# Optimization experiments

Measured on AMD Instinct MI355X. Metric: run time of the kernel, lower is better.

## Reference

```python
import jax, jax.numpy as jnp
import numpy as np

EPS = 1e-6
NEG = 0.2  # leaky-relu negative slope
OBJ_C = 6

def _knn(x, k):
    # x: [B,3,N] -> [B,N,k] indices of k nearest neighbors (incl. self)
    xx = jnp.sum(x * x, axis=1)
    inner = jnp.einsum('bdn,bdm->bnm', x, x)
    pd = 2.0 * inner - xx[:, :, None] - xx[:, None, :]  # negative sq dist
    return jax.lax.top_k(pd, k)[1]

def _gather_pts(xt, idx):
    # xt [B,N,D], idx [B,N,k] -> [B,N,k,D]
    return xt[jnp.arange(xt.shape[0])[:, None, None], idx]

def _vn_lin(W, x):
    # channel-mixing linear over VN channel dim: x [B,Cin,3,...]
    return jnp.einsum('oc,bc...->bo...', W, x)

def _vn_bn(x, g, b, eps=1e-5):
    # VNBatchNorm with batch statistics on vector norms
    n = jnp.linalg.norm(x, axis=2) + EPS          # [B,C,*spatial]
    axes = (0,) + tuple(range(2, n.ndim))
    m = jnp.mean(n, axes, keepdims=True)
    v = jnp.var(n, axes, keepdims=True)
    shp = (1, -1) + (1,) * (n.ndim - 2)
    nb = g.reshape(shp) * (n - m) / jnp.sqrt(v + eps) + b.reshape(shp)
    return x / n[:, :, None] * nb[:, :, None]

def _vn_leaky(p, d):
    dot = jnp.sum(p * d, axis=2, keepdims=True)
    dsq = jnp.sum(d * d, axis=2, keepdims=True)
    return NEG * p + (1.0 - NEG) * jnp.where(dot >= 0, p, p - (dot / (dsq + EPS)) * d)

def _vn_block(x, wf, wd, g=None, b=None):
    # VNLinearLeakyReLU
    p = _vn_lin(wf, x)
    if g is not None:
        p = _vn_bn(p, g, b)
    return _vn_leaky(p, _vn_lin(wd, x))

def _surface_feature(coord, k):
    # coord [B,3,N] -> [B,3(chan),3(vec),N,k]: (nb-ctr, ctr, nb x ctr)
    idx = _knn(coord, k)
    xt = coord.transpose(0, 2, 1)                                  # [B,N,3]
    nb = _gather_pts(xt, idx)[:, :, :, None, :]                    # [B,N,k,1,3]
    ctr = jnp.broadcast_to(xt[:, :, None, None, :], nb.shape)
    f = jnp.concatenate([nb - ctr, ctr, jnp.cross(nb, ctr, axis=-1)], axis=3)
    return f.transpose(0, 3, 4, 1, 2)

def _neighbor_feature(x, coord, k):
    # x [B,C,3,N], knn over coord -> [B,C,3,N,k]
    B, C, _, N = x.shape
    idx = _knn(coord, k)
    xt = x.reshape(B, C * 3, N).transpose(0, 2, 1)                 # [B,N,C*3]
    f = _gather_pts(xt, idx).reshape(B, N, k, C, 3)
    return f.transpose(0, 3, 4, 1, 2)

def _vn_maxpool_down(x, coord, wd, rate):
    # x [B,C,3,N,k]: stride-subsample points, VN-max over k neighbors
    x = x[:, :, :, ::rate, :]
    coord_d = coord[:, :, ::rate]
    dot = jnp.sum(x * _vn_lin(wd, x), axis=2)                      # [B,C,Nd,k]
    idx = jnp.argmax(dot, axis=-1)
    xm = jnp.take_along_axis(x, idx[:, :, None, :, None], axis=-1)[..., 0]
    return xm, coord_d

def _nearest_index(t, s):
    # t [B,N,3], s [B,M,3] -> argmin sq-dist index [B,N]
    d = jnp.sum(t * t, -1)[:, :, None] - 2.0 * jnp.einsum('bnd,bmd->bnm', t, s) + jnp.sum(s * s, -1)[:, None, :]
    return jnp.argmin(d, axis=-1)

def _index_points(x, idx):
    # x [B,C,3,M], idx [B,N] -> [B,C,3,N]
    xt = x.transpose(0, 3, 1, 2)
    return xt[jnp.arange(x.shape[0])[:, None], idx].transpose(0, 2, 3, 1)

def _conv_bn_relu(x, w, b, g, be, eps=1e-5):
    # 1x1 Conv1d + BatchNorm1d (batch stats) + ReLU
    y = jnp.einsum('oc,bcn->bon', w, x) + b[None, :, None]
    m = jnp.mean(y, (0, 2), keepdims=True)
    v = jnp.var(y, (0, 2), keepdims=True)
    return jax.nn.relu(g[None, :, None] * (y - m) / jnp.sqrt(v + eps) + be[None, :, None])

def _forward(x, norm, cat_id, wf0, wd0, g0, b0, wf1, wd1, g1, b1, wp1, wf2, wd2, g2, b2, wf3, wd3, g3, b3, wp2, wf4, wd4, g4, b4, wv1f, wv1d, wv2f, wv2d, w3, ws1, cb1, sg1, sb1, ws2, cb2, sg2, sb2, ws3, cb3, sg3, sb3):
    B, _, _, N = x.shape
    coord = x.reshape(B, 3, N)
    one_hot = jax.nn.one_hot(cat_id, OBJ_C, dtype=x.dtype)
    x0 = _vn_block(_surface_feature(coord, 20), wf0, wd0, g0, b0).mean(-1)   # [B,42,3,N]
    x1 = _vn_block(x0, wf1, wd1, g1, b1)
    x2, coord2 = _vn_maxpool_down(_neighbor_feature(x1, coord, 4), coord, wp1, 4)
    x2 = _vn_block(x2, wf2, wd2, g2, b2)                                     # [B,84,3,N/4]
    x3 = _vn_block(x2, wf3, wd3, g3, b3)
    x4, coord4 = _vn_maxpool_down(_neighbor_feature(x3, coord2, 4), coord2, wp2, 4)
    x4 = _vn_block(x4, wf4, wd4, g4, b4)                                     # [B,168,3,N/16]
    ct = coord.transpose(0, 2, 1)
    i1 = _nearest_index(ct, coord2.transpose(0, 2, 1))
    i2 = _nearest_index(ct, coord4.transpose(0, 2, 1))
    eqv = jnp.concatenate([x0, x1, _index_points(x2, i1), _index_points(x3, i1), _index_points(x4, i2)], axis=1)  # [B,420,3,N]
    mean_feat = eqv.mean(-1, keepdims=True)                                  # [B,420,3,1]
    z = _vn_block(mean_feat, wv1f, wv1d)
    z = _vn_block(z, wv2f, wv2d)
    z = jnp.einsum('bcvm,kc->bvkm', z, w3)                                   # [B,3,2,1]
    inv_gl = jnp.einsum('bijm,bjkm->bikm', mean_feat, z).reshape(B, -1, 1)   # [B,840,1]
    inv_0 = jnp.broadcast_to(inv_gl, (B, inv_gl.shape[1], N))
    inv_1 = jnp.sum(mean_feat * coord[:, None], axis=2)                      # [B,420,N]
    oh = jnp.broadcast_to(one_hot[:, :, None], (B, OBJ_C, N))
    inv = jnp.concatenate([norm, inv_0, inv_1, oh], axis=1)                  # [B,1267,N]
    inv = _conv_bn_relu(inv, ws1, cb1, sg1, sb1)
    inv = _conv_bn_relu(inv, ws2, cb2, sg2, sb2)
    inv = _conv_bn_relu(inv, ws3, cb3, sg3, sb3)                             # [B,420,N]
    return eqv, mean_feat, inv, inv_gl

def setup_inputs():
    key = jax.random.key(0)
    ki = iter(jax.random.split(key, 40))
    B, N, D = 4, 2048, 42
    def lin(o, c):
        return jax.random.normal(next(ki), (o, c), jnp.float32) / float(np.sqrt(c))
    inp = dict(
        x=jax.random.normal(next(ki), (B, 1, 3, N), jnp.float32),
        norm=jax.random.normal(next(ki), (B, 1, N), jnp.float32),
        cat_id=jax.random.randint(next(ki), (B,), 0, OBJ_C),
        wf0=lin(D, 3), wd0=lin(D, 3), g0=jnp.ones(D), b0=jnp.zeros(D),
        wf1=lin(D, D), wd1=lin(D, D), g1=jnp.ones(D), b1=jnp.zeros(D),
        wp1=lin(D, D),
        wf2=lin(2 * D, D), wd2=lin(2 * D, D), g2=jnp.ones(2 * D), b2=jnp.zeros(2 * D),
        wf3=lin(2 * D, 2 * D), wd3=lin(2 * D, 2 * D), g3=jnp.ones(2 * D), b3=jnp.zeros(2 * D),
        wp2=lin(2 * D, 2 * D),
        wf4=lin(4 * D, 2 * D), wd4=lin(4 * D, 2 * D), g4=jnp.ones(4 * D), b4=jnp.zeros(4 * D),
        wv1f=lin(5 * D, 10 * D), wv1d=lin(5 * D, 10 * D),
        wv2f=lin(2 * D, 5 * D), wv2d=lin(2 * D, 5 * D),
        w3=lin(2, 2 * D),
        ws1=lin(1024, 1267), cb1=jnp.zeros(1024), sg1=jnp.ones(1024), sb1=jnp.zeros(1024),
        ws2=lin(512, 1024), cb2=jnp.zeros(512), sg2=jnp.ones(512), sb2=jnp.zeros(512),
        ws3=lin(420, 512), cb3=jnp.zeros(420), sg3=jnp.ones(420), sb3=jnp.zeros(420),
    )
    return inp

def reference(x, norm, cat_id, wf0, wd0, g0, b0, wf1, wd1, g1, b1, wp1, wf2, wd2, g2, b2, wf3, wd3, g3, b3, wp2, wf4, wd4, g4, b4, wv1f, wv1d, wv2f, wv2d, w3, ws1, cb1, sg1, sb1, ws2, cb2, sg2, sb2, ws3, cb3, sg3, sb3):
    return _forward(x, norm, cat_id, wf0, wd0, g0, b0, wf1, wd1, g1, b1, wp1, wf2, wd2, g2, b2, wf3, wd3, g3, b3, wp2, wf4, wd4, g4, b4, wv1f, wv1d, wv2f, wv2d, w3, ws1, cb1, sg1, sb1, ws2, cb2, sg2, sb2, ws3, cb3, sg3, sb3)
```

## Files before the change

kernel.cpp:

```cpp
#include <hip/hip_runtime.h>
#include <hip/hip_bf16.h>
#include <cstdint>
#include <cstddef>

#define NTOT 2048
#define BTOT 4

typedef short bf16x8 __attribute__((ext_vector_type(8)));
typedef float f32x4 __attribute__((ext_vector_type(4)));

__device__ inline unsigned short f2b(float v) {
    __hip_bfloat16 h = __float2bfloat16(v);
    return *reinterpret_cast<unsigned short*>(&h);
}

static const size_t WS_IDX20 = 0;
static const size_t WS_X0    = 1638400;
static const size_t WS_X1    = 3702784;
static const size_t WS_XM2   = 5767168;
static const size_t WS_X2    = 6025216;
static const size_t WS_X3    = 6541312;
static const size_t WS_IDX42 = 7057408;
static const size_t WS_XM4   = 7059456;
static const size_t WS_X4    = 7188480;
static const size_t WS_I1    = 7446528;
static const size_t WS_I2    = 7454720;
static const size_t WS_MF    = 7462912;
static const size_t WS_INVGL = 7467952;
static const size_t WS_STATS = 7471312;
static const size_t WS_CST   = 7472992;
static const size_t WS_CB    = 7480320;
static const size_t WS_AB    = 7484416;
static const size_t WS_W0    = 7496704;
static const size_t WS_Z1    = 7497728;
static const size_t WS_Z2    = 7500288;
static const size_t WS_W2B   = 13378560;
static const size_t WS_W3B   = 13640704;
static const size_t WS_Y1B   = 0;
static const size_t WS_Y2T   = 7480320;
static const size_t WS_Y2B   = 4194304;
static const size_t WS_Y3T   = 13771776;

#define ST0_OFF 0
#define ST1_OFF 84
#define ST2_OFF 168
#define ST3_OFF 336
#define ST4_OFF 504
#define CST1_OFF 0
#define CST2_OFF 2048
#define CST3_OFF 3072

#define OUT_EQV   0
#define OUT_MF    10321920
#define OUT_INV   10326960
#define OUT_INVGL 13767600

template <int SLOTS, int K, int NQ>
__global__ __launch_bounds__(256)
void knn_reg_kernel(const float* __restrict__ coord, int cand_stride, int q_stride,
                    int* __restrict__ out_idx, int q_cnt)
{
#pragma clang fp contract(off)
    constexpr int Q = SLOTS / 8;
    int b = blockIdx.y;
    int wave = threadIdx.x >> 6, lane = threadIdx.x & 63;
    int qbase = (blockIdx.x * 4 + wave) * NQ;
    if (qbase >= q_cnt) return;
    float qx[NQ], qy[NQ], qz[NQ], xxq[NQ];
#pragma unroll
    for (int u = 0; u < NQ; ++u) {
        int nq = (qbase + u) * q_stride;
        qx[u] = coord[(b * 3 + 0) * NTOT + nq];
        qy[u] = coord[(b * 3 + 1) * NTOT + nq];
        qz[u] = coord[(b * 3 + 2) * NTOT + nq];
        xxq[u] = qx[u] * qx[u] + qy[u] * qy[u] + qz[u] * qz[u];
    }
    float v[NQ][SLOTS];
#pragma unroll
    for (int j = 0; j < SLOTS; ++j) {
        int mo = (lane + 64 * j) * cand_stride;
        float cx = coord[(b * 3 + 0) * NTOT + mo];
        float cy = coord[(b * 3 + 1) * NTOT + mo];
        float cz = coord[(b * 3 + 2) * NTOT + mo];
        float xxc = cx * cx + cy * cy + cz * cz;
#pragma unroll
        for (int u = 0; u < NQ; ++u) {
            float inner = qx[u] * cx + qy[u] * cy + qz[u] * cz;
            v[u][j] = (2.0f * inner - xxq[u]) - xxc;
        }
    }
    float qv[NQ][Q]; int qj[NQ][Q];
#pragma unroll
    for (int u = 0; u < NQ; ++u)
#pragma unroll
        for (int qq = 0; qq < Q; ++qq) {
            float nv = v[u][qq * 8]; int nj = qq * 8;
#pragma unroll
            for (int j = 1; j < 8; ++j)
                if (v[u][qq * 8 + j] > nv) { nv = v[u][qq * 8 + j]; nj = qq * 8 + j; }
            qv[u][qq] = nv; qj[u][qq] = nj;
        }
#pragma clang loop unroll(disable)
    for (int kk = 0; kk < K; ++kk) {
        float bv[NQ]; int bm[NQ];
#pragma unroll
        for (int u = 0; u < NQ; ++u) {
            float tv = qv[u][0]; int tj = qj[u][0];
#pragma unroll
            for (int qq = 1; qq < Q; ++qq)
                if (qv[u][qq] > tv) { tv = qv[u][qq]; tj = qj[u][qq]; }
            bv[u] = tv; bm[u] = lane + 64 * tj;
        }
        for (int off = 32; off; off >>= 1) {
            float ov[NQ]; int om[NQ];
#pragma unroll
            for (int u = 0; u < NQ; ++u) {
                ov[u] = __shfl_down(bv[u], off);
                om[u] = __shfl_down(bm[u], off);
            }
#pragma unroll
            for (int u = 0; u < NQ; ++u)
                if (ov[u] > bv[u] || (ov[u] == bv[u] && om[u] < bm[u])) {
                    bv[u] = ov[u]; bm[u] = om[u];
                }
        }
#pragma unroll
        for (int u = 0; u < NQ; ++u) {
            int m_win = __builtin_amdgcn_readfirstlane(bm[u]);
            if (lane == 0)
                out_idx[((size_t)(b * q_cnt) + qbase + u) * K + kk] = m_win;
            int w_slot = m_win >> 6;
            bool isw = (lane == (m_win & 63));
#pragma unroll
            for (int qq = 0; qq < Q; ++qq) {
                if (qq == (w_slot >> 3)) {
#pragma unroll
                    for (int j = 0; j < 8; ++j)
                        if (qq * 8 + j == w_slot)
                            v[u][qq * 8 + j] = isw ? -3.4e38f : v[u][qq * 8 + j];
                    float nv = v[u][qq * 8]; int nj = qq * 8;
#pragma unroll
                    for (int j = 1; j < 8; ++j)
                        if (v[u][qq * 8 + j] > nv) { nv = v[u][qq * 8 + j]; nj = qq * 8 + j; }
                    qv[u][qq] = nv; qj[u][qq] = nj;
                }
            }
        }
    }
}

template <int SLOTS>
__global__ __launch_bounds__(256)
void nearest_reg_kernel(const float* __restrict__ coord, int cand_stride,
                        int* __restrict__ out)
{
#pragma clang fp contract(off)
    int b = blockIdx.y;
    int wave = threadIdx.x >> 6, lane = threadIdx.x & 63;
    int n = blockIdx.x * 4 + wave;
    float qx = coord[(b * 3 + 0) * NTOT + n];
    float qy = coord[(b * 3 + 1) * NTOT + n];
    float qz = coord[(b * 3 + 2) * NTOT + n];
    float tt = qx * qx + qy * qy + qz * qz;
    float v[SLOTS];
#pragma unroll
    for (int j = 0; j < SLOTS; ++j) {
        int mo = (lane + 64 * j) * cand_stride;
        float cx = coord[(b * 3 + 0) * NTOT + mo];
        float cy = coord[(b * 3 + 1) * NTOT + mo];
        float cz = coord[(b * 3 + 2) * NTOT + mo];
        float inner = qx * cx + qy * cy + qz * cz;
        float ss = cx * cx + cy * cy + cz * cz;
        v[j] = (tt - 2.0f * inner) + ss;
    }
    float bv = v[0];
    int bj = 0;
#pragma unroll
    for (int j = 1; j < SLOTS; ++j)
        if (v[j] < bv) { bv = v[j]; bj = j; }
    int bm = lane + 64 * bj;
    for (int off = 32; off; off >>= 1) {
        float ov = __shfl_down(bv, off);
        int   om = __shfl_down(bm, off);
        if (ov < bv || (ov == bv && om < bm)) { bv = ov; bm = om; }
    }
    if (lane == 0) out[b * NTOT + n] = bm;
}

__global__ __launch_bounds__(256)
void stats0_kernel(const float* __restrict__ coord, const int* __restrict__ idx20,
                   const float* __restrict__ wf0, double* __restrict__ stats)
{
    __shared__ float nbc[360];
    __shared__ float ctr[18];
    __shared__ double red[2][6][42];
    int t = threadIdx.x, b = blockIdx.y;
    int ps = t / 42, o = t - ps * 42;
    bool active = ps < 6;
    float w0 = 0.f, w1 = 0.f, w2 = 0.f;
    if (active) { w0 = wf0[o * 3]; w1 = wf0[o * 3 + 1]; w2 = wf0[o * 3 + 2]; }
    double s = 0.0, s2 = 0.0;
    int base = blockIdx.x * 48;
    for (int it = 0; it < 8; ++it) {
        int n0 = base + it * 6;
        __syncthreads();
        if (t < 120) {
            int pl = t / 20, k = t - pl * 20;
            int n = n0 + pl; if (n > NTOT - 1) n = NTOT - 1;
            int m = idx20[((size_t)(b * NTOT + n)) * 20 + k];
            nbc[t * 3 + 0] = coord[(b * 3 + 0) * NTOT + m];
            nbc[t * 3 + 1] = coord[(b * 3 + 1) * NTOT + m];
            nbc[t * 3 + 2] = coord[(b * 3 + 2) * NTOT + m];
        }
        if (t >= 128 && t < 146) {
            int i = t - 128; int pl = i / 3, vd = i - pl * 3;
            int n = n0 + pl; if (n > NTOT - 1) n = NTOT - 1;
            ctr[i] = coord[(b * 3 + vd) * NTOT + n];
        }
        __syncthreads();
        if (active && n0 + ps < NTOT) {
            float cx = ctr[ps * 3], cy = ctr[ps * 3 + 1], cz = ctr[ps * 3 + 2];
            const float* nb = &nbc[ps * 60];
            for (int k = 0; k < 20; ++k) {
                float nx = nb[k * 3], ny = nb[k * 3 + 1], nz = nb[k * 3 + 2];
                float dx = nx - cx, dy = ny - cy, dz = nz - cz;
                float crx = ny * cz - nz * cy;
                float cry = nz * cx - nx * cz;
                float crz = nx * cy - ny * cx;
                float p0 = w0 * dx + w1 * cx + w2 * crx;
                float p1 = w0 * dy + w1 * cy + w2 * cry;
                float p2 = w0 * dz + w1 * cz + w2 * crz;
                float nrm = sqrtf(p0 * p0 + p1 * p1 + p2 * p2) + 1e-6f;
                s += (double)nrm; s2 += (double)nrm * (double)nrm;
            }
        }
    }
    if (active) { red[0][ps][o] = s; red[1][ps][o] = s2; }
    __syncthreads();
    if (t < 42) {
        double a = 0.0, a2 = 0.0;
#pragma unroll
        for (int p = 0; p < 6; ++p) { a += red[0][p][t]; a2 += red[1][p][t]; }
        atomicAdd(&stats[t], a);
        atomicAdd(&stats[42 + t], a2);
    }
}

__global__ __launch_bounds__(256)
void apply0_kernel(const float* __restrict__ coord, const int* __restrict__ idx20,
                   const float* __restrict__ wf0, const float* __restrict__ wd0,
                   const float* __restrict__ g0, const float* __restrict__ b0,
                   const double* __restrict__ stats, float* __restrict__ x0)
{
    __shared__ float nbc[360];
    __shared__ float ctr[18];
    int t = threadIdx.x;
    int b = blockIdx.y;
    int ps = t / 42, o = t - ps * 42;
    int n0 = blockIdx.x * 6;
    if (t < 120) {
        int pl = t / 20, k = t - pl * 20;
        int n = n0 + pl; if (n > NTOT - 1) n = NTOT - 1;
        int m = idx20[((size_t)(b * NTOT + n)) * 20 + k];
        nbc[t * 3 + 0] = coord[(b * 3 + 0) * NTOT + m];
        nbc[t * 3 + 1] = coord[(b * 3 + 1) * NTOT + m];
        nbc[t * 3 + 2] = coord[(b * 3 + 2) * NTOT + m];
    }
    if (t >= 128 && t < 146) {
        int i = t - 128; int pl = i / 3, vd = i - pl * 3;
        int n = n0 + pl; if (n > NTOT - 1) n = NTOT - 1;
        ctr[i] = coord[(b * 3 + vd) * NTOT + n];
    }
    __syncthreads();
    int n = n0 + ps;
    if (ps >= 6 || n >= NTOT) return;
    double S1 = stats[o], S2 = stats[42 + o];
    double md = S1 / 163840.0;
    float m = (float)md;
    float var = (float)(S2 / 163840.0 - md * md);
    float gs = g0[o] / sqrtf(var + 1e-5f);
    float bb = b0[o];
    float wa0 = wf0[o * 3], wa1 = wf0[o * 3 + 1], wa2 = wf0[o * 3 + 2];
    float wb0 = wd0[o * 3], wb1 = wd0[o * 3 + 1], wb2 = wd0[o * 3 + 2];
    float cx = ctr[ps * 3], cy = ctr[ps * 3 + 1], cz = ctr[ps * 3 + 2];
    const float* nb = &nbc[ps * 60];
    float a0 = 0.f, a1 = 0.f, a2 = 0.f;
    for (int k = 0; k < 20; ++k) {
        float nx = nb[k * 3], ny = nb[k * 3 + 1], nz = nb[k * 3 + 2];
        float dx = nx - cx, dy = ny - cy, dz = nz - cz;
        float crx = ny * cz - nz * cy;
        float cry = nz * cx - nx * cz;
        float crz = nx * cy - ny * cx;
        float p0 = wa0 * dx + wa1 * cx + wa2 * crx;
        float p1 = wa0 * dy + wa1 * cy + wa2 * cry;
        float p2 = wa0 * dz + wa1 * cz + wa2 * crz;
        float d0 = wb0 * dx + wb1 * cx + wb2 * crx;
        float d1 = wb0 * dy + wb1 * cy + wb2 * cry;
        float d2 = wb0 * dz + wb1 * cz + wb2 * crz;
        float nrm = sqrtf(p0 * p0 + p1 * p1 + p2 * p2) + 1e-6f;
        float nbv = gs * (nrm - m) + bb;
        float sc = nbv / nrm;
        p0 *= sc; p1 *= sc; p2 *= sc;
        float dot = p0 * d0 + p1 * d1 + p2 * d2;
        float dsq = d0 * d0 + d1 * d1 + d2 * d2 + 1e-6f;
        float tq = fminf(dot, 0.f) / dsq;
        a0 += 0.2f * p0 + 0.8f * (p0 - tq * d0);
        a1 += 0.2f * p1 + 0.8f * (p1 - tq * d1);
        a2 += 0.2f * p2 + 0.8f * (p2 - tq * d2);
    }
    x0[((size_t)(b * 42 + o) * 3 + 0) * NTOT + n] = a0 / 20.0f;
    x0[((size_t)(b * 42 + o) * 3 + 1) * NTOT + n] = a1 / 20.0f;
    x0[((size_t)(b * 42 + o) * 3 + 2) * NTOT + n] = a2 / 20.0f;
}

template <int Ci, int Co, int PTS, int NT, int NIT>
__global__ __launch_bounds__(NT)
void vn_stats_kernel(const float* __restrict__ xin,
                     const float* __restrict__ wf,
                     double* __restrict__ stats, int Npts)
{
    constexpr int Ci3 = Ci * 3;
    constexpr int STRIDE = Ci3 + 1;
    __shared__ float col[PTS * STRIDE];
    __shared__ double red[2][PTS][Co];
    int t = threadIdx.x;
    int b = blockIdx.y;
    int ps = t / Co;
    int o = t - ps * Co;
    bool active = ps < PTS;
    double s = 0.0, s2 = 0.0;
    int base = blockIdx.x * (PTS * NIT);
    for (int it = 0; it < NIT; ++it) {
        int pt0 = base + it * PTS;
        __syncthreads();
        for (int i = t; i < PTS * Ci3; i += NT) {
            int pl = i / Ci3, off = i - pl * Ci3;
            int pt = pt0 + pl; if (pt >= Npts) pt = Npts - 1;
            col[pl * STRIDE + off] = xin[(size_t)(b * 3 * Ci + off) * Npts + pt];
        }
        __syncthreads();
        if (active && pt0 + ps < Npts) {
            const float* cl = &col[ps * STRIDE];
            const float* wr = wf + o * Ci;
            float p0 = 0.f, p1 = 0.f, p2 = 0.f;
#pragma unroll
            for (int c = 0; c < Ci; ++c) {
                float w = wr[c];
                p0 += w * cl[3 * c]; p1 += w * cl[3 * c + 1]; p2 += w * cl[3 * c + 2];
            }
            float nrm = sqrtf(p0 * p0 + p1 * p1 + p2 * p2) + 1e-6f;
            s += (double)nrm; s2 += (double)nrm * (double)nrm;
        }
    }
    if (active) { red[0][ps][o] = s; red[1][ps][o] = s2; }
    __syncthreads();
    if (t < Co) {
        double a = 0.0, a2 = 0.0;
#pragma unroll
        for (int p = 0; p < PTS; ++p) { a += red[0][p][t]; a2 += red[1][p][t]; }
        atomicAdd(&stats[t], a);
        atomicAdd(&stats[Co + t], a2);
    }
}

template <int Ci, int Co, int PTS, int NT>
__global__ __launch_bounds__(NT)
void vn_apply_kernel(const float* __restrict__ xin,
                     const float* __restrict__ wf,
                     const float* __restrict__ wd,
                     const float* __restrict__ g,
                     const float* __restrict__ bbp,
                     const double* __restrict__ stats,
                     double count, int Npts,
                     float* __restrict__ xout)
{
    constexpr int Ci3 = Ci * 3;
    constexpr int STRIDE = Ci3 + 1;
    __shared__ float col[PTS * STRIDE];
    int t = threadIdx.x;
    int b = blockIdx.y;
    int ps = t / Co;
    int o = t - ps * Co;
    bool active = ps < PTS;
    float m = 0.f, gs = 0.f, bb = 0.f;
    if (active) {
        double S1 = stats[o], S2 = stats[Co + o];
        double md = S1 / count;
        m = (float)md;
        float var = (float)(S2 / count - md * md);
        gs = g[o] / sqrtf(var + 1e-5f);
        bb = bbp[o];
    }
    int pt0 = blockIdx.x * PTS;
    for (int i = t; i < PTS * Ci3; i += NT) {
        int pl = i / Ci3, off = i - pl * Ci3;
        int pt = pt0 + pl; if (pt >= Npts) pt = Npts - 1;
        col[pl * STRIDE + off] = xin[(size_t)(b * 3 * Ci + off) * Npts + pt];
    }
    __syncthreads();
    int pt = pt0 + ps;
    if (!active || pt >= Npts) return;
    const float* cl = &col[ps * STRIDE];
    const float* wr = wf + o * Ci;
    const float* wdr = wd + o * Ci;
    float p0 = 0.f, p1 = 0.f, p2 = 0.f, d0 = 0.f, d1 = 0.f, d2 = 0.f;
#pragma unroll
    for (int c = 0; c < Ci; ++c) {
        float c0 = cl[3 * c], c1 = cl[3 * c + 1], c2 = cl[3 * c + 2];
        float w = wr[c];
        p0 += w * c0; p1 += w * c1; p2 += w * c2;
        float w2 = wdr[c];
        d0 += w2 * c0; d1 += w2 * c1; d2 += w2 * c2;
    }
    float nrm = sqrtf(p0 * p0 + p1 * p1 + p2 * p2) + 1e-6f;
    float nb = gs * (nrm - m) + bb;
    float sc = nb / nrm;
    p0 *= sc; p1 *= sc; p2 *= sc;
    float dot = p0 * d0 + p1 * d1 + p2 * d2;
    float dsq = d0 * d0 + d1 * d1 + d2 * d2 + 1e-6f;
    float tq = fminf(dot, 0.f) / dsq;
    float r0 = p0 - tq * d0, r1 = p1 - tq * d1, r2 = p2 - tq * d2;
    xout[((size_t)(b * Co + o) * 3 + 0) * Npts + pt] = 0.2f * p0 + 0.8f * r0;
    xout[((size_t)(b * Co + o) * 3 + 1) * Npts + pt] = 0.2f * p1 + 0.8f * r1;
    xout[((size_t)(b * Co + o) * 3 + 2) * Npts + pt] = 0.2f * p2 + 0.8f * r2;
}

__global__ void vn_pool_kernel(const float* __restrict__ xin,
                               const int* __restrict__ idx, long long sb, int sq,
                               const float* __restrict__ wp,
                               float* __restrict__ xout,
                               int C, int Np, int Nq)
{
#pragma clang fp contract(off)
    __shared__ float nb[4 * 84 * 3];
    int b = blockIdx.y;
    int q = blockIdx.x;
    const int* ir = idx + b * sb + (long long)q * sq;
    for (int kk = 0; kk < 4; ++kk) {
        int mm = ir[kk];
        for (int t = threadIdx.x; t < C * 3; t += blockDim.x)
            nb[kk * C * 3 + t] = xin[(size_t)(b * 3 * C + t) * Np + mm];
    }
    __syncthreads();
    int o = threadIdx.x;
    if (o >= C) return;
    const float* wr = wp + o * C;
    float best = -3.4e38f;
    int bk = 0;
    for (int kk = 0; kk < 4; ++kk) {
        const float* cl = &nb[kk * C * 3];
        float d0 = 0.f, d1 = 0.f, d2 = 0.f;
        for (int c = 0; c < C; ++c) {
            float w = wr[c];
            d0 += w * cl[3 * c]; d1 += w * cl[3 * c + 1]; d2 += w * cl[3 * c + 2];
        }
        float dot = cl[o * 3] * d0 + cl[o * 3 + 1] * d1 + cl[o * 3 + 2] * d2;
        if (dot > best) { best = dot; bk = kk; }
    }
    const float* cb = &nb[bk * C * 3];
    xout[((size_t)(b * C + o) * 3 + 0) * Nq + q] = cb[o * 3];
    xout[((size_t)(b * C + o) * 3 + 1) * Nq + q] = cb[o * 3 + 1];
    xout[((size_t)(b * C + o) * 3 + 2) * Nq + q] = cb[o * 3 + 2];
}

__global__ void eqv_kernel(const float* __restrict__ x0, const float* __restrict__ x1,
                           const float* __restrict__ x2, const float* __restrict__ x3,
                           const float* __restrict__ x4,
                           const int* __restrict__ i1, const int* __restrict__ i2,
                           float* __restrict__ out_eqv, float* __restrict__ mfw)
{
    __shared__ float r1[256];
    int n = blockIdx.x * 256 + threadIdx.x;
    int cv = blockIdx.y;
    int b = blockIdx.z;
    int cc = cv / 3, v = cv % 3;
    float val;
    if (cc < 42)
        val = x0[((size_t)(b * 42 + cc) * 3 + v) * NTOT + n];
    else if (cc < 84)
        val = x1[((size_t)(b * 42 + (cc - 42)) * 3 + v) * NTOT + n];
    else if (cc < 168) {
        int m = i1[b * NTOT + n];
        val = x2[((size_t)(b * 84 + (cc - 84)) * 3 + v) * 512 + m];
    } else if (cc < 252) {
        int m = i1[b * NTOT + n];
        val = x3[((size_t)(b * 84 + (cc - 168)) * 3 + v) * 512 + m];
    } else {
        int m = i2[b * NTOT + n];
        val = x4[((size_t)(b * 168 + (cc - 252)) * 3 + v) * 128 + m];
    }
    out_eqv[((size_t)(b * 1260 + cv)) * NTOT + n] = val;
    r1[threadIdx.x] = val;
    __syncthreads();
    for (int off = 128; off; off >>= 1) {
        if ((int)threadIdx.x < off) r1[threadIdx.x] += r1[threadIdx.x + off];
        __syncthreads();
    }
    if (threadIdx.x == 0) atomicAdd(&mfw[b * 1260 + cv], r1[0]);
}

__global__ void mf_finalize_kernel(float* __restrict__ mfw, float* __restrict__ out_mf)
{
    int i = blockIdx.x * 256 + threadIdx.x;
    if (i < 5040) {
        float m = mfw[i] / 2048.0f;
        mfw[i] = m;
        out_mf[i] = m;
    }
}

__global__ __launch_bounds__(256)
void z1_kernel(const float* __restrict__ mfw,
               const float* __restrict__ wv1f, const float* __restrict__ wv1d,
               float* __restrict__ z1ws)
{
    __shared__ float mf[1260];
    int b = blockIdx.y;
    int wave = threadIdx.x >> 6, lane = threadIdx.x & 63;
    for (int i = threadIdx.x; i < 1260; i += 256) mf[i] = mfw[b * 1260 + i];
    __syncthreads();
    int o = blockIdx.x * 4 + wave;
    if (o >= 210) return;
    const float* wr  = wv1f + (size_t)o * 420;
    const float* wdr = wv1d + (size_t)o * 420;
    float p0 = 0.f, p1 = 0.f, p2 = 0.f, d0 = 0.f, d1 = 0.f, d2 = 0.f;
    for (int c = lane; c < 420; c += 64) {
        float m0 = mf[3 * c], m1 = mf[3 * c + 1], m2 = mf[3 * c + 2];
        float w = wr[c];
        p0 += w * m0; p1 += w * m1; p2 += w * m2;
        float w2 = wdr[c];
        d0 += w2 * m0; d1 += w2 * m1; d2 += w2 * m2;
    }
    for (int off = 32; off; off >>= 1) {
        p0 += __shfl_down(p0, off); p1 += __shfl_down(p1, off);
        p2 += __shfl_down(p2, off); d0 += __shfl_down(d0, off);
        d1 += __shfl_down(d1, off); d2 += __shfl_down(d2, off);
    }
    if (lane == 0) {
        float dot = p0 * d0 + p1 * d1 + p2 * d2;
        float r0, r1, r2;
        if (dot >= 0.f) { r0 = p0; r1 = p1; r2 = p2; }
        else {
            float tq = dot / (d0 * d0 + d1 * d1 + d2 * d2 + 1e-6f);
            r0 = p0 - tq * d0; r1 = p1 - tq * d1; r2 = p2 - tq * d2;
        }
        z1ws[b * 630 + o * 3]     = 0.2f * p0 + 0.8f * r0;
        z1ws[b * 630 + o * 3 + 1] = 0.2f * p1 + 0.8f * r1;
        z1ws[b * 630 + o * 3 + 2] = 0.2f * p2 + 0.8f * r2;
    }
}

__global__ __launch_bounds__(256)
void z2_kernel(const float* __restrict__ z1ws,
               const float* __restrict__ wv2f, const float* __restrict__ wv2d,
               float* __restrict__ z2ws)
{
    __shared__ float zl[630];
    int b = blockIdx.y;
    int wave = threadIdx.x >> 6, lane = threadIdx.x & 63;
    for (int i = threadIdx.x; i < 630; i += 256) zl[i] = z1ws[b * 630 + i];
    __syncthreads();
    int o = blockIdx.x * 4 + wave;
    if (o >= 84) return;
    const float* wr  = wv2f + (size_t)o * 210;
    const float* wdr = wv2d + (size_t)o * 210;
    float p0 = 0.f, p1 = 0.f, p2 = 0.f, d0 = 0.f, d1 = 0.f, d2 = 0.f;
    for (int c = lane; c < 210; c += 64) {
        float m0 = zl[3 * c], m1 = zl[3 * c + 1], m2 = zl[3 * c + 2];
        float w = wr[c];
        p0 += w * m0; p1 += w * m1; p2 += w * m2;
        float w2 = wdr[c];
        d0 += w2 * m0; d1 += w2 * m1; d2 += w2 * m2;
    }
    for (int off = 32; off; off >>= 1) {
        p0 += __shfl_down(p0, off); p1 += __shfl_down(p1, off);
        p2 += __shfl_down(p2, off); d0 += __shfl_down(d0, off);
        d1 += __shfl_down(d1, off); d2 += __shfl_down(d2, off);
    }
    if (lane == 0) {
        float dot = p0 * d0 + p1 * d1 + p2 * d2;
        float r0, r1, r2;
        if (dot >= 0.f) { r0 = p0; r1 = p1; r2 = p2; }
        else {
            float tq = dot / (d0 * d0 + d1 * d1 + d2 * d2 + 1e-6f);
            r0 = p0 - tq * d0; r1 = p1 - tq * d1; r2 = p2 - tq * d2;
        }
        z2ws[b * 252 + o * 3]     = 0.2f * p0 + 0.8f * r0;
        z2ws[b * 252 + o * 3 + 1] = 0.2f * p1 + 0.8f * r1;
        z2ws[b * 252 + o * 3 + 2] = 0.2f * p2 + 0.8f * r2;
    }
}

__global__ void z3invgl_kernel(const float* __restrict__ mfw,
                               const float* __restrict__ z2ws,
                               const float* __restrict__ w3,
                               float* __restrict__ invgl_ws,
                               float* __restrict__ out_invgl)
{
    __shared__ float z2[252];
    __shared__ float z3[6];
    __shared__ float mf[1260];
    int b = blockIdx.x;
    int t = threadIdx.x;
    for (int i = t; i < 252; i += 256) z2[i] = z2ws[b * 252 + i];
    for (int i = t; i < 1260; i += 256) mf[i] = mfw[b * 1260 + i];
    __syncthreads();
    if (t < 6) {
        int v = t / 2, kt = t % 2;
        float s = 0.f;
        for (int c = 0; c < 84; ++c) s += z2[c * 3 + v] * w3[kt * 84 + c];
        z3[v * 2 + kt] = s;
    }
    __syncthreads();
    for (int i = t; i < 840; i += 256) {
        int ii = i / 2, kt = i % 2;
        float s = mf[ii * 3] * z3[0 + kt] + mf[ii * 3 + 1] * z3[2 + kt] +
                  mf[ii * 3 + 2] * z3[4 + kt];
        invgl_ws[b * 840 + i] = s;
        out_invgl[b * 840 + i] = s;
    }
}

__global__ __launch_bounds__(256)
void conv1_coef_kernel(const float* __restrict__ ws1,
                       const float* __restrict__ invgl,
                       const float* __restrict__ mfw,
                       const int* __restrict__ cat,
                       float* __restrict__ cb, float* __restrict__ ab,
                       float* __restrict__ w0)
{
    int wave = threadIdx.x >> 6, lane = threadIdx.x & 63;
    int o = blockIdx.x * 4 + wave;
    int b = blockIdx.y;
    const float* wr = ws1 + (size_t)o * 1267;
    float s = 0.f;
    for (int j = lane; j < 840; j += 64)
        s += wr[1 + j] * invgl[b * 840 + j];
    float a0 = 0.f, a1 = 0.f, a2 = 0.f;
    for (int i = lane; i < 420; i += 64) {
        float w = wr[841 + i];
        a0 += w * mfw[b * 1260 + i * 3];
        a1 += w * mfw[b * 1260 + i * 3 + 1];
        a2 += w * mfw[b * 1260 + i * 3 + 2];
    }
    for (int off = 32; off; off >>= 1) {
        s  += __shfl_down(s, off);
        a0 += __shfl_down(a0, off);
        a1 += __shfl_down(a1, off);
        a2 += __shfl_down(a2, off);
    }
    if (lane == 0) {
        cb[b * 1024 + o] = s + wr[1261 + cat[b]];
        ab[((size_t)(b * 1024 + o)) * 3 + 0] = a0;
        ab[((size_t)(b * 1024 + o)) * 3 + 1] = a1;
        ab[((size_t)(b * 1024 + o)) * 3 + 2] = a2;
        if (b == 0) w0[o] = wr[0];
    }
}

__global__ __launch_bounds__(256)
void y1_stats_kernel(const float* __restrict__ cb, const float* __restrict__ ab,
                     const float* __restrict__ w0, const float* __restrict__ coord,
                     const float* __restrict__ normv, float* __restrict__ cst)
{
    __shared__ float px[256], py[256], pz[256], pn[256];
    int t = threadIdx.x;
    int o = blockIdx.x * 256 + t;
    int b = blockIdx.y >> 3;
    int n0 = (blockIdx.y & 7) * 256;
    px[t] = coord[(b * 3 + 0) * NTOT + n0 + t];
    py[t] = coord[(b * 3 + 1) * NTOT + n0 + t];
    pz[t] = coord[(b * 3 + 2) * NTOT + n0 + t];
    pn[t] = normv[b * NTOT + n0 + t];
    __syncthreads();
    size_t bo = (size_t)(b * 1024 + o);
    float c0 = cb[bo];
    float a0 = ab[bo * 3], a1 = ab[bo * 3 + 1], a2 = ab[bo * 3 + 2];
    float wn = w0[o];
    float s = 0.f, s2 = 0.f;
    for (int k = 0; k < 256; ++k) {
        float v = c0 + a0 * px[k] + a1 * py[k] + a2 * pz[k] + wn * pn[k];
        s += v; s2 += v * v;
    }
    atomicAdd(&cst[o], s);
    atomicAdd(&cst[1024 + o], s2);
}

__global__ __launch_bounds__(256)
void y1_bnrelu_kernel(const float* __restrict__ cb, const float* __restrict__ ab,
                      const float* __restrict__ w0, const float* __restrict__ coord,
                      const float* __restrict__ normv, const float* __restrict__ cst,
                      const float* __restrict__ sg, const float* __restrict__ sb,
                      unsigned short* __restrict__ y1b)
{
    __shared__ float px[256], py[256], pz[256], pn[256];
    int t = threadIdx.x;
    int o = blockIdx.x * 256 + t;
    int b = blockIdx.y >> 3;
    int n0 = (blockIdx.y & 7) * 256;
    px[t] = coord[(b * 3 + 0) * NTOT + n0 + t];
    py[t] = coord[(b * 3 + 1) * NTOT + n0 + t];
    pz[t] = coord[(b * 3 + 2) * NTOT + n0 + t];
    pn[t] = normv[b * NTOT + n0 + t];
    __syncthreads();
    size_t bo = (size_t)(b * 1024 + o);
    float c0 = cb[bo];
    float a0 = ab[bo * 3], a1 = ab[bo * 3 + 1], a2 = ab[bo * 3 + 2];
    float wn = w0[o];
    float mm = cst[o] * (1.f / 8192.f);
    float var = cst[1024 + o] * (1.f / 8192.f) - mm * mm;
    float sc = sg[o] / sqrtf(var + 1e-5f);
    float bs = sb[o] - mm * sc;
    size_t rowbase = (size_t)(b * NTOT + n0) * 1024 + o;
    for (int k = 0; k < 256; ++k) {
        float v = c0 + a0 * px[k] + a1 * py[k] + a2 * pz[k] + wn * pn[k];
        float r = sc * v + bs;
        y1b[rowbase + (size_t)k * 1024] = f2b(r > 0.f ? r : 0.f);
    }
}

__global__ void wconv_kernel(const float* __restrict__ src, unsigned short* __restrict__ dst,
                             int Msrc, int Ksrc, int Kpad)
{
    int k = blockIdx.x * 256 + threadIdx.x;
    int o = blockIdx.y;
    float v = (o < Msrc && k < Ksrc) ? src[(size_t)o * Ksrc + k] : 0.f;
    dst[(size_t)o * Kpad + k] = f2b(v);
}

__global__ __launch_bounds__(256)
void gemm_mfma_kernel(const unsigned short* __restrict__ A,
                      const unsigned short* __restrict__ Bw,
                      float* __restrict__ C, float* __restrict__ st,
                      int K, int Mreal)
{
    __shared__ __align__(16) unsigned short Al[128 * 40];
    __shared__ __align__(16) unsigned short Bl[128 * 40];
    __shared__ float sst[128], sst2[128];
    int t = threadIdx.x;
    if (t < 128) { sst[t] = 0.f; sst2[t] = 0.f; }
    int r0 = blockIdx.x * 128;
    int c0 = blockIdx.y * 128;
    int w = t >> 6, l = t & 63;
    int wm = w & 1, wn = w >> 1;
    int lm = l & 15, lq = l >> 4;
    f32x4 acc[4][4] = {};
    for (int k0 = 0; k0 < K; k0 += 32) {
        for (int half = 0; half < 2; ++half) {
            int ch = t + half * 256;
            int row = ch >> 2, kc = ch & 3;
            *(uint4*)&Al[row * 40 + kc * 8] =
                *(const uint4*)&A[(size_t)(r0 + row) * K + k0 + kc * 8];
            *(uint4*)&Bl[row * 40 + kc * 8] =
                *(const uint4*)&Bw[(size_t)(c0 + row) * K + k0 + kc * 8];
        }
        __syncthreads();
        bf16x8 af[4], bfr[4];
#pragma unroll
        for (int i = 0; i < 4; ++i)
            af[i] = *(const bf16x8*)&Al[(wm * 64 + i * 16 + lm) * 40 + lq * 8];
#pragma unroll
        for (int j = 0; j < 4; ++j)
            bfr[j] = *(const bf16x8*)&Bl[(wn * 64 + j * 16 + lm) * 40 + lq * 8];
#pragma unroll
        for (int i = 0; i < 4; ++i)
#pragma unroll
            for (int j = 0; j < 4; ++j)
                acc[i][j] = __builtin_amdgcn_mfma_f32_16x16x32_bf16(af[i], bfr[j],
                                                                    acc[i][j], 0, 0, 0);
        __syncthreads();
    }
#pragma unroll
    for (int i = 0; i < 4; ++i) {
#pragma unroll
        for (int j = 0; j < 4; ++j) {
            int col = c0 + wn * 64 + j * 16 + lm;
            if (col < Mreal) {
                int rbase = r0 + wm * 64 + i * 16 + lq * 4;
#pragma unroll
                for (int r = 0; r < 4; ++r)
                    C[(size_t)(rbase + r) * Mreal + col] = acc[i][j][r];
            }
        }
    }
#pragma unroll
    for (int j = 0; j < 4; ++j) {
        float s = 0.f, s2 = 0.f;
#pragma unroll
        for (int i = 0; i < 4; ++i)
#pragma unroll
            for (int r = 0; r < 4; ++r) { float x = acc[i][j][r]; s += x; s2 += x * x; }
        s  += __shfl_down(s, 32);  s  += __shfl_down(s, 16);
        s2 += __shfl_down(s2, 32); s2 += __shfl_down(s2, 16);
        if (l < 16) {
            int cc = wn * 64 + j * 16 + lm;
            atomicAdd(&sst[cc], s);
            atomicAdd(&sst2[cc], s2);
        }
    }
    __syncthreads();
    if (t < 128) {
        int col = c0 + t;
        if (col < Mreal) {
            atomicAdd(&st[col], sst[t]);
            atomicAdd(&st[Mreal + col], sst2[t]);
        }
    }
}

__global__ void bnreluT_kernel(const float* __restrict__ Ct, const float* __restrict__ st,
                               const float* __restrict__ g, const float* __restrict__ be,
                               unsigned short* __restrict__ outb, int M, int maskM)
{
    size_t idx = (size_t)blockIdx.x * 256 + threadIdx.x;
    int o = (int)(idx & (size_t)maskM);
    float m = st[o] * (1.f / 8192.f);
    float var = st[M + o] * (1.f / 8192.f) - m * m;
    float sqv = sqrtf(var + 1e-5f);
    float v = g[o] * (Ct[idx] - m) / sqv + be[o];
    outb[idx] = f2b(v > 0.f ? v : 0.f);
}

__global__ void bnrelu_outT_kernel(const float* __restrict__ Ct, const float* __restrict__ st,
                                   const float* __restrict__ g, const float* __restrict__ be,
                                   float* __restrict__ outinv)
{
    __shared__ float tile[64][65];
    int t = threadIdx.x;
    int r0 = blockIdx.x * 64;
    int o0 = blockIdx.y * 64;
    int b = r0 >> 11, n0 = r0 & 2047;
    int oi = t & 63;
    int o = o0 + oi;
    float m = 0.f, sqv = 1.f, gg = 0.f, bb = 0.f;
    if (o < 420) {
        m = st[o] * (1.f / 8192.f);
        float var = st[420 + o] * (1.f / 8192.f) - m * m;
        sqv = sqrtf(var + 1e-5f);
        gg = g[o]; bb = be[o];
    }
    for (int it = 0; it < 16; ++it) {
        int rr = it * 4 + (t >> 6);
        float v = 0.f;
        if (o < 420) {
            v = gg * (Ct[(size_t)(r0 + rr) * 420 + o] - m) / sqv + bb;
            v = v > 0.f ? v : 0.f;
        }
        tile[rr][oi] = v;
    }
    __syncthreads();
    for (int it = 0; it < 16; ++it) {
        int oc = it * 4 + (t >> 6);
        int oo = o0 + oc;
        if (oo < 420)
            outinv[((size_t)(b * 420 + oo)) * 2048 + n0 + (t & 63)] = tile[t & 63][oc];
    }
}

extern "C" void kernel_launch(void* const* d_in, const int* in_sizes, int n_in,
                              void* d_out, int out_size, void* d_ws, size_t ws_size,
                              hipStream_t stream)
{
    (void)in_sizes; (void)n_in; (void)out_size; (void)ws_size;
    const float* xc   = (const float*)d_in[0];
    const float* normv= (const float*)d_in[1];
    const int*   cat  = (const int*)d_in[2];
    const float* wf0  = (const float*)d_in[3];
    const float* wd0  = (const float*)d_in[4];
    const float* g0   = (const float*)d_in[5];
    const float* b0   = (const float*)d_in[6];
    const float* wf1  = (const float*)d_in[7];
    const float* wd1  = (const float*)d_in[8];
    const float* g1   = (const float*)d_in[9];
    const float* b1   = (const float*)d_in[10];
    const float* wp1  = (const float*)d_in[11];
    const float* wf2  = (const float*)d_in[12];
    const float* wd2  = (const float*)d_in[13];
    const float* g2   = (const float*)d_in[14];
    const float* b2   = (const float*)d_in[15];
    const float* wf3  = (const float*)d_in[16];
    const float* wd3  = (const float*)d_in[17];
    const float* g3   = (const float*)d_in[18];
    const float* b3   = (const float*)d_in[19];
    const float* wp2  = (const float*)d_in[20];
    const float* wf4  = (const float*)d_in[21];
    const float* wd4  = (const float*)d_in[22];
    const float* g4   = (const float*)d_in[23];
    const float* b4   = (const float*)d_in[24];
    const float* wv1f = (const float*)d_in[25];
    const float* wv1d = (const float*)d_in[26];
    const float* wv2f = (const float*)d_in[27];
    const float* wv2d = (const float*)d_in[28];
    const float* w3   = (const float*)d_in[29];
    const float* ws1  = (const float*)d_in[30];
    const float* sg1  = (const float*)d_in[32];
    const float* sb1  = (const float*)d_in[33];
    const float* ws2  = (const float*)d_in[34];
    const float* sg2  = (const float*)d_in[36];
    const float* sb2  = (const float*)d_in[37];
    const float* ws3  = (const float*)d_in[38];
    const float* sg3  = (const float*)d_in[40];
    const float* sb3  = (const float*)d_in[41];

    float* ws = (float*)d_ws;
    float* out = (float*)d_out;

    int*    idx20 = (int*)(ws + WS_IDX20);
    float*  x0    = ws + WS_X0;
    float*  x1    = ws + WS_X1;
    float*  xm2   = ws + WS_XM2;
    float*  x2    = ws + WS_X2;
    float*  x3    = ws + WS_X3;
    int*    idx42 = (int*)(ws + WS_IDX42);
    float*  xm4   = ws + WS_XM4;
    float*  x4    = ws + WS_X4;
    int*    i1p   = (int*)(ws + WS_I1);
    int*    i2p   = (int*)(ws + WS_I2);
    float*  mfw   = ws + WS_MF;
    float*  invgl = ws + WS_INVGL;
    double* st    = (double*)(ws + WS_STATS);
    float*  cst   = ws + WS_CST;
    float*  cb    = ws + WS_CB;
    float*  ab    = ws + WS_AB;
    float*  w0    = ws + WS_W0;
    float*  z1ws  = ws + WS_Z1;
    float*  z2ws  = ws + WS_Z2;
    unsigned short* w2b  = (unsigned short*)(ws + WS_W2B);
    unsigned short* w3b  = (unsigned short*)(ws + WS_W3B);
    unsigned short* y1b  = (unsigned short*)(ws + WS_Y1B);
    float*  y2t   = ws + WS_Y2T;
    unsigned short* y2b  = (unsigned short*)(ws + WS_Y2B);
    float*  y3t   = ws + WS_Y3T;

    hipMemsetAsync((void*)st, 0, 840 * sizeof(double), stream);
    hipMemsetAsync((void*)cst, 0, 3912 * sizeof(float), stream);
    hipMemsetAsync((void*)mfw, 0, 5040 * sizeof(float), stream);

    wconv_kernel<<<dim3(4, 512), 256, 0, stream>>>(ws2, w2b, 512, 1024, 1024);
    wconv_kernel<<<dim3(2, 512), 256, 0, stream>>>(ws3, w3b, 420, 512, 512);

    knn_reg_kernel<32, 20, 2><<<dim3(256, 4), 256, 0, stream>>>(xc, 1, 1, idx20, 2048);

    stats0_kernel<<<dim3(43, 4), 256, 0, stream>>>(xc, idx20, wf0, st + ST0_OFF);
    apply0_kernel<<<dim3(342, 4), 256, 0, stream>>>(xc, idx20, wf0, wd0, g0, b0,
                                                    st + ST0_OFF, x0);

    vn_stats_kernel<42, 42, 6, 256, 8><<<dim3(43, 4), 256, 0, stream>>>(
        x0, wf1, st + ST1_OFF, 2048);
    vn_apply_kernel<42, 42, 6, 256><<<dim3(342, 4), 256, 0, stream>>>(
        x0, wf1, wd1, g1, b1, st + ST1_OFF, 8192.0, 2048, x1);

    vn_pool_kernel<<<dim3(512, 4), 256, 0, stream>>>(x1, idx20, 40960LL, 80, wp1, xm2,
                                                     42, 2048, 512);
    vn_stats_kernel<42, 84, 3, 256, 8><<<dim3(22, 4), 256, 0, stream>>>(
        xm2, wf2, st + ST2_OFF, 512);
    vn_apply_kernel<42, 84, 3, 256><<<dim3(171, 4), 256, 0, stream>>>(
        xm2, wf2, wd2, g2, b2, st + ST2_OFF, 2048.0, 512, x2);
    vn_stats_kernel<84, 84, 3, 256, 8><<<dim3(22, 4), 256, 0, stream>>>(
        x2, wf3, st + ST3_OFF, 512);
    vn_apply_kernel<84, 84, 3, 256><<<dim3(171, 4), 256, 0, stream>>>(
        x2, wf3, wd3, g3, b3, st + ST3_OFF, 2048.0, 512, x3);

    knn_reg_kernel<8, 4, 1><<<dim3(32, 4), 256, 0, stream>>>(xc, 4, 16, idx42, 128);
    vn_pool_kernel<<<dim3(128, 4), 256, 0, stream>>>(x3, idx42, 512LL, 4, wp2, xm4,
                                                     84, 512, 128);
    vn_stats_kernel<84, 168, 3, 512, 4><<<dim3(11, 4), 512, 0, stream>>>(
        xm4, wf4, st + ST4_OFF, 128);
    vn_apply_kernel<84, 168, 3, 512><<<dim3(43, 4), 512, 0, stream>>>(
        xm4, wf4, wd4, g4, b4, st + ST4_OFF, 512.0, 128, x4);

    nearest_reg_kernel<8><<<dim3(512, 4), 256, 0, stream>>>(xc, 4, i1p);
    nearest_reg_kernel<2><<<dim3(512, 4), 256, 0, stream>>>(xc, 16, i2p);

    eqv_kernel<<<dim3(8, 1260, 4), 256, 0, stream>>>(x0, x1, x2, x3, x4, i1p, i2p,
                                                     out + OUT_EQV, mfw);
    mf_finalize_kernel<<<20, 256, 0, stream>>>(mfw, out + OUT_MF);

    z1_kernel<<<dim3(53, 4), 256, 0, stream>>>(mfw, wv1f, wv1d, z1ws);
    z2_kernel<<<dim3(21, 4), 256, 0, stream>>>(z1ws, wv2f, wv2d, z2ws);
    z3invgl_kernel<<<4, 256, 0, stream>>>(mfw, z2ws, w3, invgl, out + OUT_INVGL);

    conv1_coef_kernel<<<dim3(256, 4), 256, 0, stream>>>(ws1, invgl, mfw, cat, cb, ab, w0);
    y1_stats_kernel<<<dim3(4, 32), 256, 0, stream>>>(cb, ab, w0, xc, normv,
                                                     cst + CST1_OFF);
    y1_bnrelu_kernel<<<dim3(4, 32), 256, 0, stream>>>(cb, ab, w0, xc, normv,
                                                      cst + CST1_OFF, sg1, sb1, y1b);

    gemm_mfma_kernel<<<dim3(64, 4), 256, 0, stream>>>(y1b, w2b, y2t, cst + CST2_OFF,
                                                      1024, 512);
    bnreluT_kernel<<<16384, 256, 0, stream>>>(y2t, cst + CST2_OFF, sg2, sb2, y2b,
                                              512, 511);

    gemm_mfma_kernel<<<dim3(64, 4), 256, 0, stream>>>(y2b, w3b, y3t, cst + CST3_OFF,
                                                      512, 420);
    bnrelu_outT_kernel<<<dim3(128, 7), 256, 0, stream>>>(y3t, cst + CST3_OFF, sg3, sb3,
                                                         out + OUT_INV);
}
```

Before: 631.0 us.

## Shrink GEMM tiles to 64x64 with K=64, use warp-shuffle reduction, merge memsets

The MFMA GEMM tile drops from 128x128 to 64x64 with a 64-wide K step, and the grid grows to 128x8 and 128x7 blocks. This gives more blocks to fill the many compute units on the small GEMMs, at the cost of less data reuse per tile. The eqv kernel's shared-memory tree reduction is replaced with wavefront shuffles plus a 4-entry shared array, cutting the number of barriers. The three workspace memsets are merged into one contiguous memset that starts at mfw; this relies on stats, cst and mfw being adjacent in the workspace layout.

```diff
diff --git a/kernel.cpp b/kernel.cpp
--- a/kernel.cpp
+++ b/kernel.cpp
@@ -40,6 +40,8 @@
 static const size_t WS_Y2T   = 7480320;
 static const size_t WS_Y2B   = 4194304;
 static const size_t WS_Y3T   = 13771776;
+
+#define ZERO_SPAN_BYTES ((7476904 - 7462912) * 4)
 
 #define ST0_OFF 0
 #define ST1_OFF 84
@@ -469,7 +471,7 @@
                            const int* __restrict__ i1, const int* __restrict__ i2,
                            float* __restrict__ out_eqv, float* __restrict__ mfw)
 {
-    __shared__ float r1[256];
+    __shared__ float wsum[4];
     int n = blockIdx.x * 256 + threadIdx.x;
     int cv = blockIdx.y;
     int b = blockIdx.z;
@@ -490,13 +492,12 @@
         val = x4[((size_t)(b * 168 + (cc - 252)) * 3 + v) * 128 + m];
     }
     out_eqv[((size_t)(b * 1260 + cv)) * NTOT + n] = val;
-    r1[threadIdx.x] = val;
-    __syncthreads();
-    for (int off = 128; off; off >>= 1) {
-        if ((int)threadIdx.x < off) r1[threadIdx.x] += r1[threadIdx.x + off];
-        __syncthreads();
-    }
-    if (threadIdx.x == 0) atomicAdd(&mfw[b * 1260 + cv], r1[0]);
+    float s = val;
+    for (int off = 32; off; off >>= 1) s += __shfl_down(s, off);
+    if ((threadIdx.x & 63) == 0) wsum[threadIdx.x >> 6] = s;
+    __syncthreads();
+    if (threadIdx.x == 0)
+        atomicAdd(&mfw[b * 1260 + cv], (wsum[0] + wsum[1]) + (wsum[2] + wsum[3]));
 }
 
 __global__ void mf_finalize_kernel(float* __restrict__ mfw, float* __restrict__ out_mf)
@@ -734,49 +735,55 @@
                       float* __restrict__ C, float* __restrict__ st,
                       int K, int Mreal)
 {
-    __shared__ __align__(16) unsigned short Al[128 * 40];
-    __shared__ __align__(16) unsigned short Bl[128 * 40];
-    __shared__ float sst[128], sst2[128];
+    __shared__ __align__(16) unsigned short Al[64 * 72];
+    __shared__ __align__(16) unsigned short Bl[64 * 72];
+    __shared__ float sst[64], sst2[64];
     int t = threadIdx.x;
-    if (t < 128) { sst[t] = 0.f; sst2[t] = 0.f; }
-    int r0 = blockIdx.x * 128;
-    int c0 = blockIdx.y * 128;
+    if (t < 64) { sst[t] = 0.f; sst2[t] = 0.f; }
+    int r0 = blockIdx.x * 64;
+    int c0 = blockIdx.y * 64;
     int w = t >> 6, l = t & 63;
     int wm = w & 1, wn = w >> 1;
     int lm = l & 15, lq = l >> 4;
-    f32x4 acc[4][4] = {};
-    for (int k0 = 0; k0 < K; k0 += 32) {
+    f32x4 acc[2][2] = {};
+    for (int k0 = 0; k0 < K; k0 += 64) {
+#pragma unroll
         for (int half = 0; half < 2; ++half) {
             int ch = t + half * 256;
-            int row = ch >> 2, kc = ch & 3;
-            *(uint4*)&Al[row * 40 + kc * 8] =
+            int row = ch >> 3, kc = ch & 7;
+            *(uint4*)&Al[row * 72 + kc * 8] =
                 *(const uint4*)&A[(size_t)(r0 + row) * K + k0 + kc * 8];
-            *(uint4*)&Bl[row * 40 + kc * 8] =
+            *(uint4*)&Bl[row * 72 + kc * 8] =
                 *(const uint4*)&Bw[(size_t)(c0 + row) * K + k0 + kc * 8];
         }
         __syncthreads();
-        bf16x8 af[4], bfr[4];
-#pragma unroll
-        for (int i = 0; i < 4; ++i)
-            af[i] = *(const bf16x8*)&Al[(wm * 64 + i * 16 + lm) * 40 + lq * 8];
-#pragma unroll
-        for (int j = 0; j < 4; ++j)
-            bfr[j] = *(const bf16x8*)&Bl[(wn * 64 + j * 16 + lm) * 40 + lq * 8];
-#pragma unroll
-        for (int i = 0; i < 4; ++i)
-#pragma unroll
-            for (int j = 0; j < 4; ++j)
-                acc[i][j] = __builtin_amdgcn_mfma_f32_16x16x32_bf16(af[i], bfr[j],
-                                                                    acc[i][j], 0, 0, 0);
+        bf16x8 af[2][2], bfr[2][2];
+#pragma unroll
+        for (int kk = 0; kk < 2; ++kk) {
+#pragma unroll
+            for (int i = 0; i < 2; ++i)
+                af[kk][i] = *(const bf16x8*)&Al[(wm * 32 + i * 16 + lm) * 72 + kk * 32 + lq * 8];
+#pragma unroll
+            for (int j = 0; j < 2; ++j)
+                bfr[kk][j] = *(const bf16x8*)&Bl[(wn * 32 + j * 16 + lm) * 72 + kk * 32 + lq * 8];
+        }
+#pragma unroll
+        for (int kk = 0; kk < 2; ++kk)
+#pragma unroll
+            for (int i = 0; i < 2; ++i)
+#pragma unroll
+                for (int j = 0; j < 2; ++j)
+                    acc[i][j] = __builtin_amdgcn_mfma_f32_16x16x32_bf16(
+                        af[kk][i], bfr[kk][j], acc[i][j], 0, 0, 0);
         __syncthreads();
     }
 #pragma unroll
-    for (int i = 0; i < 4; ++i) {
-#pragma unroll
-        for (int j = 0; j < 4; ++j) {
-            int col = c0 + wn * 64 + j * 16 + lm;
+    for (int i = 0; i < 2; ++i) {
+#pragma unroll
+        for (int j = 0; j < 2; ++j) {
+            int col = c0 + wn * 32 + j * 16 + lm;
             if (col < Mreal) {
-                int rbase = r0 + wm * 64 + i * 16 + lq * 4;
+                int rbase = r0 + wm * 32 + i * 16 + lq * 4;
 #pragma unroll
                 for (int r = 0; r < 4; ++r)
                     C[(size_t)(rbase + r) * Mreal + col] = acc[i][j][r];
@@ -784,22 +791,22 @@
         }
     }
 #pragma unroll
-    for (int j = 0; j < 4; ++j) {
+    for (int j = 0; j < 2; ++j) {
         float s = 0.f, s2 = 0.f;
 #pragma unroll
-        for (int i = 0; i < 4; ++i)
+        for (int i = 0; i < 2; ++i)
 #pragma unroll
             for (int r = 0; r < 4; ++r) { float x = acc[i][j][r]; s += x; s2 += x * x; }
         s  += __shfl_down(s, 32);  s  += __shfl_down(s, 16);
         s2 += __shfl_down(s2, 32); s2 += __shfl_down(s2, 16);
         if (l < 16) {
-            int cc = wn * 64 + j * 16 + lm;
+            int cc = wn * 32 + j * 16 + lm;
             atomicAdd(&sst[cc], s);
             atomicAdd(&sst2[cc], s2);
         }
     }
     __syncthreads();
-    if (t < 128) {
+    if (t < 64) {
         int col = c0 + t;
         if (col < Mreal) {
             atomicAdd(&st[col], sst[t]);
@@ -932,9 +939,7 @@
     unsigned short* y2b  = (unsigned short*)(ws + WS_Y2B);
     float*  y3t   = ws + WS_Y3T;
 
-    hipMemsetAsync((void*)st, 0, 840 * sizeof(double), stream);
-    hipMemsetAsync((void*)cst, 0, 3912 * sizeof(float), stream);
-    hipMemsetAsync((void*)mfw, 0, 5040 * sizeof(float), stream);
+    hipMemsetAsync((void*)mfw, 0, ZERO_SPAN_BYTES, stream);
 
     wconv_kernel<<<dim3(4, 512), 256, 0, stream>>>(ws2, w2b, 512, 1024, 1024);
     wconv_kernel<<<dim3(2, 512), 256, 0, stream>>>(ws3, w3b, 420, 512, 512);
@@ -986,13 +991,13 @@
     y1_bnrelu_kernel<<<dim3(4, 32), 256, 0, stream>>>(cb, ab, w0, xc, normv,
                                                       cst + CST1_OFF, sg1, sb1, y1b);
 
-    gemm_mfma_kernel<<<dim3(64, 4), 256, 0, stream>>>(y1b, w2b, y2t, cst + CST2_OFF,
-                                                      1024, 512);
+    gemm_mfma_kernel<<<dim3(128, 8), 256, 0, stream>>>(y1b, w2b, y2t, cst + CST2_OFF,
+                                                       1024, 512);
     bnreluT_kernel<<<16384, 256, 0, stream>>>(y2t, cst + CST2_OFF, sg2, sb2, y2b,
                                               512, 511);
 
-    gemm_mfma_kernel<<<dim3(64, 4), 256, 0, stream>>>(y2b, w3b, y3t, cst + CST3_OFF,
-                                                      512, 420);
+    gemm_mfma_kernel<<<dim3(128, 7), 256, 0, stream>>>(y2b, w3b, y3t, cst + CST3_OFF,
+                                                       512, 420);
     bnrelu_outT_kernel<<<dim3(128, 7), 256, 0, stream>>>(y3t, cst + CST3_OFF, sg3, sb3,
                                                          out + OUT_INV);
 }
```

Result: faster. 577.1 us (-8.5%).
